# Kernel optimization log

Measured on AMD Instinct MI355X. Metric: run time of the kernel, lower is better.

Reference implementation:

```python
import jax, jax.numpy as jnp
import numpy as np

DIM = 256
FFN_DIM = 512
NH = 8
EPS = 1e-5


def ln(x, g, b):
    m = x.mean(-1, keepdims=True)
    v = ((x - m) ** 2).mean(-1, keepdims=True)
    return (x - m) / jnp.sqrt(v + EPS) * g + b


def setup_inputs() -> dict:
    key = jax.random.key(0)
    ks = jax.random.split(key, 16)
    B, L, C, H, W = 16, 16384, DIM, 128, 128
    s = 0.02
    return {
        "query": jax.random.normal(ks[0], (B, 1, C), jnp.float32),
        "mem": jax.random.normal(ks[1], (B, L, C), jnp.float32),
        "ior_emb": jax.random.uniform(ks[2], (B, NH, H, W), jnp.float32),
        # input_proj: Linear(dim,dim) + ReLU + LayerNorm
        "W_ip": jax.random.normal(ks[3], (C, C), jnp.float32) * s,
        "b_ip": jnp.zeros((C,), jnp.float32),
        "g_ip": jnp.ones((C,), jnp.float32),
        "be_ip": jnp.zeros((C,), jnp.float32),
        # q / kv projections
        "W_q": jax.random.normal(ks[4], (C, C), jnp.float32) * s,
        "b_q": jnp.zeros((C,), jnp.float32),
        "W_kv": jax.random.normal(ks[5], (C, 2 * C), jnp.float32) * s,
        "b_kv": jnp.zeros((2 * C,), jnp.float32),
        # norm_q, norm_ffn
        "g_q": jnp.ones((C,), jnp.float32),
        "be_q": jnp.zeros((C,), jnp.float32),
        "g_f": jnp.ones((C,), jnp.float32),
        "be_f": jnp.zeros((C,), jnp.float32),
        # ffn (Mlp)
        "W1": jax.random.normal(ks[6], (C, FFN_DIM), jnp.float32) * s,
        "b1": jnp.zeros((FFN_DIM,), jnp.float32),
        "W2": jax.random.normal(ks[7], (FFN_DIM, C), jnp.float32) * s,
        "b2": jnp.zeros((C,), jnp.float32),
    }


def reference(query, mem, ior_emb, W_ip, b_ip, g_ip, be_ip, W_q, b_q, W_kv, b_kv,
              g_q, be_q, g_f, be_f, W1, b1, W2, b2):
    B, L, C = mem.shape
    nh = ior_emb.shape[1]
    hd = C // nh
    scale = hd ** -0.5
    # input_proj(mem): Linear -> ReLU -> LayerNorm
    m = ln(jax.nn.relu(mem @ W_ip + b_ip), g_ip, be_ip)  # [B,L,C]
    kv = m @ W_kv + b_kv
    k, v = kv[..., :C], kv[..., C:]
    q = ln(query, g_q, be_q) @ W_q + b_q  # [B,1,C]
    # per-head split along channel == reshape (..., nh, hd)
    qh = q.reshape(B, 1, nh, hd)
    kh = k.reshape(B, L, nh, hd)
    vh = v.reshape(B, L, nh, hd)
    ior = ior_emb.reshape(B, nh, 1, L)
    scores = jnp.einsum('bqhd,blhd->bhql', qh, kh) * scale * ior  # [B,nh,1,L]
    attn = jax.nn.softmax(scores, axis=-1)
    out = jnp.einsum('bhql,blhd->bqhd', attn, vh).reshape(B, 1, C)
    x = out + query
    h = ln(x, g_f, be_f)
    ffn = jax.nn.gelu(h @ W1 + b1, approximate=False) @ W2 + b2
    return x + ffn
```

## Files before the change

kernel.cpp:

```cpp
#include <hip/hip_runtime.h>
#include <math.h>

#define CDIM 256
#define LDIM 16384
#define NH 8
#define HD 32
#define FFN 512
#define EPS 1e-5f
#define SCALE 0.17677669529663687f

#define RB 64
#define CHUNKS (LDIM/RB)
#define LDA 264

typedef __attribute__((ext_vector_type(8))) short short8;
typedef __attribute__((ext_vector_type(4))) float f32x4;

__device__ inline unsigned short f2bf(float x) {
    unsigned int u = __float_as_uint(x);
    unsigned int lsb = (u >> 16) & 1u;
    u += 0x7fffu + lsb;
    return (unsigned short)(u >> 16);
}


__global__ __launch_bounds__(256) void convert_weights(const float* __restrict__ Wip,
                                                       const float* __restrict__ Wkv,
                                                       unsigned short* __restrict__ w1,
                                                       unsigned short* __restrict__ wkv) {
    int idx = blockIdx.x * 256 + threadIdx.x;
    if (idx < 65536) {
        int j = idx & 7, l = (idx >> 3) & 63, c = (idx >> 9) & 15, t = idx >> 13;
        int k = t * 32 + (l >> 4) * 8 + j;
        int col = c * 16 + (l & 15);
        w1[idx] = f2bf(Wip[k * CDIM + col]);
    }
    if (idx < 131072) {
        int j = idx & 7, l = (idx >> 3) & 63, c = (idx >> 9) & 31, t = idx >> 14;
        int k = t * 32 + (l >> 4) * 8 + j;
        int col = c * 16 + (l & 15);
        wkv[idx] = f2bf(Wkv[k * 2 * CDIM + col]);
    }
}


__global__ __launch_bounds__(256) void qprep_kernel(const float* __restrict__ query,
                                                    const float* __restrict__ Wq,
                                                    const float* __restrict__ bq,
                                                    const float* __restrict__ gq,
                                                    const float* __restrict__ beq,
                                                    float* __restrict__ qs) {
    int b = blockIdx.x;
    int tid = threadIdx.x;
    int wave = tid >> 6, lane = tid & 63;
    __shared__ float sh[CDIM];
    __shared__ float red[8];

    float x = query[b * CDIM + tid];
    float s = x, sq = x * x;
#pragma unroll
    for (int m = 32; m >= 1; m >>= 1) { s += __shfl_xor(s, m, 64); sq += __shfl_xor(sq, m, 64); }
    if (lane == 0) { red[wave] = s; red[4 + wave] = sq; }
    __syncthreads();
    float ts = red[0] + red[1] + red[2] + red[3];
    float tq = red[4] + red[5] + red[6] + red[7];
    float mean = ts * (1.f / CDIM);
    float var = tq * (1.f / CDIM) - mean * mean;
    float rstd = rsqrtf(var + EPS);
    sh[tid] = (x - mean) * rstd * gq[tid] + beq[tid];
    __syncthreads();

    float acc = bq[tid];
    for (int k = 0; k < CDIM; ++k) acc = fmaf(sh[k], Wq[k * CDIM + tid], acc);
    qs[b * CDIM + tid] = acc * SCALE;
}


__device__ inline void mfma_gemm(const unsigned short* __restrict__ smA,
                                 const unsigned short* __restrict__ wsw, int NC, int ctile0,
                                 int lx, int quad, f32x4 acc[4][4]) {
#pragma unroll
    for (int rt = 0; rt < 4; ++rt)
#pragma unroll
        for (int ci = 0; ci < 4; ++ci) acc[rt][ci] = (f32x4){0.f, 0.f, 0.f, 0.f};

    int l = quad * 16 + lx;
#pragma unroll
    for (int t = 0; t < 8; ++t) {
        short8 bfrag[4];
#pragma unroll
        for (int ci = 0; ci < 4; ++ci)
            bfrag[ci] = *(const short8*)(wsw + (((size_t)(t * NC + ctile0 + ci)) * 64 + l) * 8);
        short8 afrag[4];
#pragma unroll
        for (int rt = 0; rt < 4; ++rt)
            afrag[rt] = *(const short8*)(smA + (rt * 16 + lx) * LDA + t * 32 + quad * 8);
#pragma unroll
        for (int rt = 0; rt < 4; ++rt)
#pragma unroll
            for (int ci = 0; ci < 4; ++ci)
                acc[rt][ci] = __builtin_amdgcn_mfma_f32_16x16x32_bf16(afrag[rt], bfrag[ci], acc[rt][ci], 0, 0, 0);
    }
}


__global__ __launch_bounds__(256, 2) void main_kernel(const float* __restrict__ mem,
                                                      const unsigned short* __restrict__ w1,
                                                      const unsigned short* __restrict__ wkv,
                                                      const float* __restrict__ bip,
                                                      const float* __restrict__ gip,
                                                      const float* __restrict__ beip,
                                                      const float* __restrict__ bkv,
                                                      const float* __restrict__ ior,
                                                      const float* __restrict__ qs,
                                                      float* __restrict__ partials) {
    int blk = blockIdx.x;
    int b = blk / CHUNKS;
    int chunk = blk % CHUNKS;
    int row0 = chunk * RB;
    int tid = threadIdx.x;
    int w = tid >> 6, l = tid & 63;
    int quad = l >> 4, lx = l & 15;

    __shared__ unsigned short bufA[RB * LDA];
    __shared__ float iorS[NH][RB];
    __shared__ float redS[4][RB];
    __shared__ float redQ[4][RB];
    __shared__ float stats[2][RB];

    {
        int i0 = tid, i1 = tid + 256;
        int h0 = i0 >> 6, r0 = i0 & 63;
        int h1 = i1 >> 6, r1 = i1 & 63;
        iorS[h0][r0] = ior[((size_t)(b * NH + h0)) * LDIM + row0 + r0];
        iorS[h1][r1] = ior[((size_t)(b * NH + h1)) * LDIM + row0 + r1];
    }
    {
        const float4* src = (const float4*)(mem + ((size_t)b * LDIM + row0) * CDIM);
#pragma unroll
        for (int it = 0; it < 16; ++it) {
            int i = tid + 256 * it;
            int r = i >> 6, c4 = i & 63;
            float4 v = src[i];
            ushort4 u;
            u.x = f2bf(v.x); u.y = f2bf(v.y); u.z = f2bf(v.z); u.w = f2bf(v.w);
            *(ushort4*)&bufA[r * LDA + c4 * 4] = u;
        }
    }
    __syncthreads();

    int col[4];
#pragma unroll
    for (int ci = 0; ci < 4; ++ci) col[ci] = (4 * w + ci) * 16 + lx;

    f32x4 acc[4][4];
    mfma_gemm(bufA, w1, 16, 4 * w, lx, quad, acc);

    float bb[4], gg[4], ee[4];
#pragma unroll
    for (int ci = 0; ci < 4; ++ci) { bb[ci] = bip[col[ci]]; gg[ci] = gip[col[ci]]; ee[ci] = beip[col[ci]]; }

#pragma unroll
    for (int rt = 0; rt < 4; ++rt) {
#pragma unroll
        for (int reg = 0; reg < 4; ++reg) {
#pragma unroll
            for (int ci = 0; ci < 4; ++ci)
                acc[rt][ci][reg] = fmaxf(acc[rt][ci][reg] + bb[ci], 0.f);
            float s = acc[rt][0][reg] + acc[rt][1][reg] + acc[rt][2][reg] + acc[rt][3][reg];
            float q = acc[rt][0][reg] * acc[rt][0][reg] + acc[rt][1][reg] * acc[rt][1][reg]
                    + acc[rt][2][reg] * acc[rt][2][reg] + acc[rt][3][reg] * acc[rt][3][reg];
#pragma unroll
            for (int m = 8; m >= 1; m >>= 1) { s += __shfl_xor(s, m, 64); q += __shfl_xor(q, m, 64); }
            if (lx == 0) {
                int row = rt * 16 + quad * 4 + reg;
                redS[w][row] = s;
                redQ[w][row] = q;
            }
        }
    }
    __syncthreads();
    if (tid < RB) {
        float s = redS[0][tid] + redS[1][tid] + redS[2][tid] + redS[3][tid];
        float q = redQ[0][tid] + redQ[1][tid] + redQ[2][tid] + redQ[3][tid];
        float mean = s * (1.f / CDIM);
        float var = q * (1.f / CDIM) - mean * mean;
        stats[0][tid] = mean;
        stats[1][tid] = rsqrtf(var + EPS);
    }
    __syncthreads();

#pragma unroll
    for (int rt = 0; rt < 4; ++rt)
#pragma unroll
        for (int reg = 0; reg < 4; ++reg) {
            int row = rt * 16 + quad * 4 + reg;
            float mean = stats[0][row], rstd = stats[1][row];
#pragma unroll
            for (int ci = 0; ci < 4; ++ci) {
                float y = (acc[rt][ci][reg] - mean) * rstd * gg[ci] + ee[ci];
                bufA[row * LDA + col[ci]] = f2bf(y);
            }
        }
    __syncthreads();

    f32x4 acc2[4][4];
    mfma_gemm(bufA, wkv, 32, 4 * w, lx, quad, acc2);

    float qv[4], bk[4];
#pragma unroll
    for (int ci = 0; ci < 4; ++ci) { qv[ci] = qs[b * CDIM + col[ci]]; bk[ci] = bkv[col[ci]]; }

    float p0[16], p1[16];
    float M0 = -1e30f, M1 = -1e30f;
#pragma unroll
    for (int rt = 0; rt < 4; ++rt)
#pragma unroll
        for (int reg = 0; reg < 4; ++reg) {
            float s0 = (acc2[rt][0][reg] + bk[0]) * qv[0] + (acc2[rt][1][reg] + bk[1]) * qv[1];
            float s1 = (acc2[rt][2][reg] + bk[2]) * qv[2] + (acc2[rt][3][reg] + bk[3]) * qv[3];
#pragma unroll
            for (int m = 8; m >= 1; m >>= 1) { s0 += __shfl_xor(s0, m, 64); s1 += __shfl_xor(s1, m, 64); }
            int row = rt * 16 + quad * 4 + reg;
            s0 *= iorS[2 * w][row];
            s1 *= iorS[2 * w + 1][row];
            p0[rt * 4 + reg] = s0;
            p1[rt * 4 + reg] = s1;
            M0 = fmaxf(M0, s0);
            M1 = fmaxf(M1, s1);
        }
    M0 = fmaxf(M0, __shfl_xor(M0, 16, 64)); M0 = fmaxf(M0, __shfl_xor(M0, 32, 64));
    M1 = fmaxf(M1, __shfl_xor(M1, 16, 64)); M1 = fmaxf(M1, __shfl_xor(M1, 32, 64));
    float S0 = 0.f, S1 = 0.f;
#pragma unroll
    for (int i = 0; i < 16; ++i) {
        p0[i] = __expf(p0[i] - M0); S0 += p0[i];
        p1[i] = __expf(p1[i] - M1); S1 += p1[i];
    }
    S0 += __shfl_xor(S0, 16, 64); S0 += __shfl_xor(S0, 32, 64);
    S1 += __shfl_xor(S1, 16, 64); S1 += __shfl_xor(S1, 32, 64);

    f32x4 acc3[4][4];
    mfma_gemm(bufA, wkv, 32, 16 + 4 * w, lx, quad, acc3);

    float o[4];
#pragma unroll
    for (int ci = 0; ci < 4; ++ci) {
        float bo = bkv[CDIM + col[ci]];
        const float* pp = (ci < 2) ? p0 : p1;
        float a = 0.f;
#pragma unroll
        for (int rt = 0; rt < 4; ++rt)
#pragma unroll
            for (int reg = 0; reg < 4; ++reg)
                a = fmaf(pp[rt * 4 + reg], acc3[rt][ci][reg] + bo, a);
        a += __shfl_xor(a, 16, 64);
        a += __shfl_xor(a, 32, 64);
        o[ci] = a;
    }

    float* P0 = &partials[((size_t)blk * NH + 2 * w) * 34];
    float* P1 = P0 + 34;
    if (quad == 0) {
        P0[2 + lx] = o[0];
        P0[2 + 16 + lx] = o[1];
        P1[2 + lx] = o[2];
        P1[2 + 16 + lx] = o[3];
        if (lx == 0) { P0[0] = M0; P0[1] = S0; P1[0] = M1; P1[1] = S1; }
    }
}


__global__ __launch_bounds__(64) void combine_kernel(const float* __restrict__ partials,
                                                     float* __restrict__ attnout) {
    int bh = blockIdx.x;
    int b = bh >> 3, h = bh & 7;
    int lane = threadIdx.x;

    float M = -1e30f;
    for (int c = lane; c < CHUNKS; c += 64)
        M = fmaxf(M, partials[(((size_t)b * CHUNKS + c) * NH + h) * 34]);
#pragma unroll
    for (int m = 32; m >= 1; m >>= 1) M = fmaxf(M, __shfl_xor(M, m, 64));

    float S = 0.f;
    for (int c = lane; c < CHUNKS; c += 64) {
        const float* P = &partials[(((size_t)b * CHUNKS + c) * NH + h) * 34];
        S += P[1] * __expf(P[0] - M);
    }
#pragma unroll
    for (int m = 32; m >= 1; m >>= 1) S += __shfl_xor(S, m, 64);

    int d = lane & 31, half = lane >> 5;
    float O = 0.f;
    for (int c = half; c < CHUNKS; c += 2) {
        const float* P = &partials[(((size_t)b * CHUNKS + c) * NH + h) * 34];
        O = fmaf(P[2 + d], __expf(P[0] - M), O);
    }
    O += __shfl_xor(O, 32, 64);
    if (lane < 32) attnout[b * CDIM + h * HD + d] = O / S;
}


__global__ __launch_bounds__(256) void epilogue_kernel(const float* __restrict__ attnout,
                                                       const float* __restrict__ query,
                                                       const float* __restrict__ gf,
                                                       const float* __restrict__ bef,
                                                       const float* __restrict__ W1,
                                                       const float* __restrict__ b1,
                                                       const float* __restrict__ W2,
                                                       const float* __restrict__ b2,
                                                       float* __restrict__ out) {
    int b = blockIdx.x;
    int tid = threadIdx.x;
    int wave = tid >> 6, lane = tid & 63;
    __shared__ float sh[FFN];
    __shared__ float red[8];

    float x = attnout[b * CDIM + tid] + query[b * CDIM + tid];
    float s = x, sq = x * x;
#pragma unroll
    for (int m = 32; m >= 1; m >>= 1) { s += __shfl_xor(s, m, 64); sq += __shfl_xor(sq, m, 64); }
    if (lane == 0) { red[wave] = s; red[4 + wave] = sq; }
    __syncthreads();
    float ts = red[0] + red[1] + red[2] + red[3];
    float tq = red[4] + red[5] + red[6] + red[7];
    float mean = ts * (1.f / CDIM);
    float var = tq * (1.f / CDIM) - mean * mean;
    float rstd = rsqrtf(var + EPS);
    sh[tid] = (x - mean) * rstd * gf[tid] + bef[tid];
    __syncthreads();

    float t[2];
#pragma unroll
    for (int i = 0; i < 2; ++i) {
        int f = tid + 256 * i;
        float a = b1[f];
        for (int k = 0; k < CDIM; ++k) a = fmaf(sh[k], W1[k * FFN + f], a);
        t[i] = 0.5f * a * (1.f + erff(a * 0.7071067811865476f));
    }
    __syncthreads();
    sh[tid] = t[0];
    sh[tid + 256] = t[1];
    __syncthreads();

    float y = b2[tid];
    for (int f = 0; f < FFN; ++f) y = fmaf(sh[f], W2[f * CDIM + tid], y);
    out[b * CDIM + tid] = x + y;
}


extern "C" void kernel_launch(void* const* d_in, const int* in_sizes, int n_in,
                              void* d_out, int out_size, void* d_ws, size_t ws_size,
                              hipStream_t stream) {
    const float* query = (const float*)d_in[0];
    const float* mem   = (const float*)d_in[1];
    const float* ior   = (const float*)d_in[2];
    const float* Wip   = (const float*)d_in[3];
    const float* bip   = (const float*)d_in[4];
    const float* gip   = (const float*)d_in[5];
    const float* beip  = (const float*)d_in[6];
    const float* Wq    = (const float*)d_in[7];
    const float* bq    = (const float*)d_in[8];
    const float* Wkv   = (const float*)d_in[9];
    const float* bkv   = (const float*)d_in[10];
    const float* gq    = (const float*)d_in[11];
    const float* beq   = (const float*)d_in[12];
    const float* gf    = (const float*)d_in[13];
    const float* bef   = (const float*)d_in[14];
    const float* W1    = (const float*)d_in[15];
    const float* b1    = (const float*)d_in[16];
    const float* W2    = (const float*)d_in[17];
    const float* b2    = (const float*)d_in[18];
    float* out = (float*)d_out;

    char* ws = (char*)d_ws;
    float* qs             = (float*)(ws);
    float* attnout        = (float*)(ws + 16384);
    float* partials       = (float*)(ws + 32768);
    unsigned short* w1sw  = (unsigned short*)(ws + 32768 + 4456448);
    unsigned short* wkvsw = (unsigned short*)(ws + 32768 + 4456448 + 131072);

    const int B = 16;

    convert_weights<<<512, 256, 0, stream>>>(Wip, Wkv, w1sw, wkvsw);
    qprep_kernel<<<B, 256, 0, stream>>>(query, Wq, bq, gq, beq, qs);
    main_kernel<<<B * CHUNKS, 256, 0, stream>>>(mem, w1sw, wkvsw, bip, gip, beip, bkv, ior, qs, partials);
    combine_kernel<<<B * NH, 64, 0, stream>>>(partials, attnout);
    epilogue_kernel<<<B, 256, 0, stream>>>(attnout, query, gf, bef, W1, b1, W2, b2, out);
}
```

Before: 611.3 us.

## Halve rows per block, fuse K and V GEMMs, merge prep kernels

Cuts rows per block from 64 to 32, doubling the block count and raising launch bounds to 3 blocks per CU for better occupancy on the memory-bound main kernel. The K and V projection GEMMs are merged into one loop so the A fragments from shared memory are read once for both. Weight conversion and query prep are combined into one launch, and the partials workspace is doubled. The cost is that each block now reloads the full weight fragments for half as many rows, doubling weight traffic per row, and more partials have to be combined.

```diff
diff --git a/kernel.cpp b/kernel.cpp
--- a/kernel.cpp
+++ b/kernel.cpp
@@ -9,7 +9,7 @@
 #define EPS 1e-5f
 #define SCALE 0.17677669529663687f
 
-#define RB 64
+#define RB 32
 #define CHUNKS (LDIM/RB)
 #define LDA 264
 
@@ -24,87 +24,59 @@
 }
 
 
-__global__ __launch_bounds__(256) void convert_weights(const float* __restrict__ Wip,
-                                                       const float* __restrict__ Wkv,
-                                                       unsigned short* __restrict__ w1,
-                                                       unsigned short* __restrict__ wkv) {
-    int idx = blockIdx.x * 256 + threadIdx.x;
-    if (idx < 65536) {
-        int j = idx & 7, l = (idx >> 3) & 63, c = (idx >> 9) & 15, t = idx >> 13;
-        int k = t * 32 + (l >> 4) * 8 + j;
-        int col = c * 16 + (l & 15);
-        w1[idx] = f2bf(Wip[k * CDIM + col]);
-    }
-    if (idx < 131072) {
-        int j = idx & 7, l = (idx >> 3) & 63, c = (idx >> 9) & 31, t = idx >> 14;
-        int k = t * 32 + (l >> 4) * 8 + j;
-        int col = c * 16 + (l & 15);
-        wkv[idx] = f2bf(Wkv[k * 2 * CDIM + col]);
-    }
-}
-
-
-__global__ __launch_bounds__(256) void qprep_kernel(const float* __restrict__ query,
-                                                    const float* __restrict__ Wq,
-                                                    const float* __restrict__ bq,
-                                                    const float* __restrict__ gq,
-                                                    const float* __restrict__ beq,
-                                                    float* __restrict__ qs) {
-    int b = blockIdx.x;
-    int tid = threadIdx.x;
-    int wave = tid >> 6, lane = tid & 63;
-    __shared__ float sh[CDIM];
-    __shared__ float red[8];
-
-    float x = query[b * CDIM + tid];
-    float s = x, sq = x * x;
-#pragma unroll
-    for (int m = 32; m >= 1; m >>= 1) { s += __shfl_xor(s, m, 64); sq += __shfl_xor(sq, m, 64); }
-    if (lane == 0) { red[wave] = s; red[4 + wave] = sq; }
-    __syncthreads();
-    float ts = red[0] + red[1] + red[2] + red[3];
-    float tq = red[4] + red[5] + red[6] + red[7];
-    float mean = ts * (1.f / CDIM);
-    float var = tq * (1.f / CDIM) - mean * mean;
-    float rstd = rsqrtf(var + EPS);
-    sh[tid] = (x - mean) * rstd * gq[tid] + beq[tid];
-    __syncthreads();
-
-    float acc = bq[tid];
-    for (int k = 0; k < CDIM; ++k) acc = fmaf(sh[k], Wq[k * CDIM + tid], acc);
-    qs[b * CDIM + tid] = acc * SCALE;
-}
-
-
-__device__ inline void mfma_gemm(const unsigned short* __restrict__ smA,
-                                 const unsigned short* __restrict__ wsw, int NC, int ctile0,
-                                 int lx, int quad, f32x4 acc[4][4]) {
-#pragma unroll
-    for (int rt = 0; rt < 4; ++rt)
-#pragma unroll
-        for (int ci = 0; ci < 4; ++ci) acc[rt][ci] = (f32x4){0.f, 0.f, 0.f, 0.f};
-
-    int l = quad * 16 + lx;
-#pragma unroll
-    for (int t = 0; t < 8; ++t) {
-        short8 bfrag[4];
-#pragma unroll
-        for (int ci = 0; ci < 4; ++ci)
-            bfrag[ci] = *(const short8*)(wsw + (((size_t)(t * NC + ctile0 + ci)) * 64 + l) * 8);
-        short8 afrag[4];
-#pragma unroll
-        for (int rt = 0; rt < 4; ++rt)
-            afrag[rt] = *(const short8*)(smA + (rt * 16 + lx) * LDA + t * 32 + quad * 8);
-#pragma unroll
-        for (int rt = 0; rt < 4; ++rt)
-#pragma unroll
-            for (int ci = 0; ci < 4; ++ci)
-                acc[rt][ci] = __builtin_amdgcn_mfma_f32_16x16x32_bf16(afrag[rt], bfrag[ci], acc[rt][ci], 0, 0, 0);
-    }
-}
-
-
-__global__ __launch_bounds__(256, 2) void main_kernel(const float* __restrict__ mem,
+__global__ __launch_bounds__(256) void prep_kernel(const float* __restrict__ Wip,
+                                                   const float* __restrict__ Wkv,
+                                                   unsigned short* __restrict__ w1,
+                                                   unsigned short* __restrict__ wkv,
+                                                   const float* __restrict__ query,
+                                                   const float* __restrict__ Wq,
+                                                   const float* __restrict__ bq,
+                                                   const float* __restrict__ gq,
+                                                   const float* __restrict__ beq,
+                                                   float* __restrict__ qs) {
+    if (blockIdx.x < 512) {
+        int idx = blockIdx.x * 256 + threadIdx.x;
+        if (idx < 65536) {
+            int j = idx & 7, l = (idx >> 3) & 63, c = (idx >> 9) & 15, t = idx >> 13;
+            int k = t * 32 + (l >> 4) * 8 + j;
+            int col = c * 16 + (l & 15);
+            w1[idx] = f2bf(Wip[k * CDIM + col]);
+        }
+        {
+            int j = idx & 7, l = (idx >> 3) & 63, c = (idx >> 9) & 31, t = idx >> 14;
+            int k = t * 32 + (l >> 4) * 8 + j;
+            int col = c * 16 + (l & 15);
+            wkv[idx] = f2bf(Wkv[k * 2 * CDIM + col]);
+        }
+    } else {
+        int b = blockIdx.x - 512;
+        int tid = threadIdx.x;
+        int wave = tid >> 6, lane = tid & 63;
+        __shared__ float sh[CDIM];
+        __shared__ float red[8];
+
+        float x = query[b * CDIM + tid];
+        float s = x, sq = x * x;
+#pragma unroll
+        for (int m = 32; m >= 1; m >>= 1) { s += __shfl_xor(s, m, 64); sq += __shfl_xor(sq, m, 64); }
+        if (lane == 0) { red[wave] = s; red[4 + wave] = sq; }
+        __syncthreads();
+        float ts = red[0] + red[1] + red[2] + red[3];
+        float tq = red[4] + red[5] + red[6] + red[7];
+        float mean = ts * (1.f / CDIM);
+        float var = tq * (1.f / CDIM) - mean * mean;
+        float rstd = rsqrtf(var + EPS);
+        sh[tid] = (x - mean) * rstd * gq[tid] + beq[tid];
+        __syncthreads();
+
+        float acc = bq[tid];
+        for (int k = 0; k < CDIM; ++k) acc = fmaf(sh[k], Wq[k * CDIM + tid], acc);
+        qs[b * CDIM + tid] = acc * SCALE;
+    }
+}
+
+
+__global__ __launch_bounds__(256, 3) void main_kernel(const float* __restrict__ mem,
                                                       const unsigned short* __restrict__ w1,
                                                       const unsigned short* __restrict__ wkv,
                                                       const float* __restrict__ bip,
@@ -129,16 +101,13 @@
     __shared__ float stats[2][RB];
 
     {
-        int i0 = tid, i1 = tid + 256;
-        int h0 = i0 >> 6, r0 = i0 & 63;
-        int h1 = i1 >> 6, r1 = i1 & 63;
+        int h0 = tid >> 5, r0 = tid & 31;
         iorS[h0][r0] = ior[((size_t)(b * NH + h0)) * LDIM + row0 + r0];
-        iorS[h1][r1] = ior[((size_t)(b * NH + h1)) * LDIM + row0 + r1];
     }
     {
         const float4* src = (const float4*)(mem + ((size_t)b * LDIM + row0) * CDIM);
 #pragma unroll
-        for (int it = 0; it < 16; ++it) {
+        for (int it = 0; it < 8; ++it) {
             int i = tid + 256 * it;
             int r = i >> 6, c4 = i & 63;
             float4 v = src[i];
@@ -153,15 +122,34 @@
 #pragma unroll
     for (int ci = 0; ci < 4; ++ci) col[ci] = (4 * w + ci) * 16 + lx;
 
-    f32x4 acc[4][4];
-    mfma_gemm(bufA, w1, 16, 4 * w, lx, quad, acc);
+    f32x4 acc[2][4];
+#pragma unroll
+    for (int rt = 0; rt < 2; ++rt)
+#pragma unroll
+        for (int ci = 0; ci < 4; ++ci) acc[rt][ci] = (f32x4){0.f, 0.f, 0.f, 0.f};
+#pragma unroll
+    for (int t = 0; t < 8; ++t) {
+        short8 bfrag[4];
+#pragma unroll
+        for (int ci = 0; ci < 4; ++ci)
+            bfrag[ci] = *(const short8*)(w1 + (((size_t)(t * 16 + 4 * w + ci)) * 64 + l) * 8);
+        short8 afrag[2];
+#pragma unroll
+        for (int rt = 0; rt < 2; ++rt)
+            afrag[rt] = *(const short8*)(bufA + (rt * 16 + lx) * LDA + t * 32 + quad * 8);
+#pragma unroll
+        for (int rt = 0; rt < 2; ++rt)
+#pragma unroll
+            for (int ci = 0; ci < 4; ++ci)
+                acc[rt][ci] = __builtin_amdgcn_mfma_f32_16x16x32_bf16(afrag[rt], bfrag[ci], acc[rt][ci], 0, 0, 0);
+    }
 
     float bb[4], gg[4], ee[4];
 #pragma unroll
     for (int ci = 0; ci < 4; ++ci) { bb[ci] = bip[col[ci]]; gg[ci] = gip[col[ci]]; ee[ci] = beip[col[ci]]; }
 
 #pragma unroll
-    for (int rt = 0; rt < 4; ++rt) {
+    for (int rt = 0; rt < 2; ++rt) {
 #pragma unroll
         for (int reg = 0; reg < 4; ++reg) {
 #pragma unroll
@@ -191,7 +179,7 @@
     __syncthreads();
 
 #pragma unroll
-    for (int rt = 0; rt < 4; ++rt)
+    for (int rt = 0; rt < 2; ++rt)
 #pragma unroll
         for (int reg = 0; reg < 4; ++reg) {
             int row = rt * 16 + quad * 4 + reg;
@@ -204,17 +192,43 @@
         }
     __syncthreads();
 
-    f32x4 acc2[4][4];
-    mfma_gemm(bufA, wkv, 32, 4 * w, lx, quad, acc2);
+    f32x4 acc2[2][4], acc3[2][4];
+#pragma unroll
+    for (int rt = 0; rt < 2; ++rt)
+#pragma unroll
+        for (int ci = 0; ci < 4; ++ci) {
+            acc2[rt][ci] = (f32x4){0.f, 0.f, 0.f, 0.f};
+            acc3[rt][ci] = (f32x4){0.f, 0.f, 0.f, 0.f};
+        }
+#pragma unroll
+    for (int t = 0; t < 8; ++t) {
+        short8 bfragK[4], bfragV[4];
+#pragma unroll
+        for (int ci = 0; ci < 4; ++ci) {
+            bfragK[ci] = *(const short8*)(wkv + (((size_t)(t * 32 + 4 * w + ci)) * 64 + l) * 8);
+            bfragV[ci] = *(const short8*)(wkv + (((size_t)(t * 32 + 16 + 4 * w + ci)) * 64 + l) * 8);
+        }
+        short8 afrag[2];
+#pragma unroll
+        for (int rt = 0; rt < 2; ++rt)
+            afrag[rt] = *(const short8*)(bufA + (rt * 16 + lx) * LDA + t * 32 + quad * 8);
+#pragma unroll
+        for (int rt = 0; rt < 2; ++rt)
+#pragma unroll
+            for (int ci = 0; ci < 4; ++ci) {
+                acc2[rt][ci] = __builtin_amdgcn_mfma_f32_16x16x32_bf16(afrag[rt], bfragK[ci], acc2[rt][ci], 0, 0, 0);
+                acc3[rt][ci] = __builtin_amdgcn_mfma_f32_16x16x32_bf16(afrag[rt], bfragV[ci], acc3[rt][ci], 0, 0, 0);
+            }
+    }
 
     float qv[4], bk[4];
 #pragma unroll
     for (int ci = 0; ci < 4; ++ci) { qv[ci] = qs[b * CDIM + col[ci]]; bk[ci] = bkv[col[ci]]; }
 
-    float p0[16], p1[16];
+    float p0[8], p1[8];
     float M0 = -1e30f, M1 = -1e30f;
 #pragma unroll
-    for (int rt = 0; rt < 4; ++rt)
+    for (int rt = 0; rt < 2; ++rt)
 #pragma unroll
         for (int reg = 0; reg < 4; ++reg) {
             float s0 = (acc2[rt][0][reg] + bk[0]) * qv[0] + (acc2[rt][1][reg] + bk[1]) * qv[1];
@@ -233,15 +247,12 @@
     M1 = fmaxf(M1, __shfl_xor(M1, 16, 64)); M1 = fmaxf(M1, __shfl_xor(M1, 32, 64));
     float S0 = 0.f, S1 = 0.f;
 #pragma unroll
-    for (int i = 0; i < 16; ++i) {
+    for (int i = 0; i < 8; ++i) {
         p0[i] = __expf(p0[i] - M0); S0 += p0[i];
         p1[i] = __expf(p1[i] - M1); S1 += p1[i];
     }
     S0 += __shfl_xor(S0, 16, 64); S0 += __shfl_xor(S0, 32, 64);
     S1 += __shfl_xor(S1, 16, 64); S1 += __shfl_xor(S1, 32, 64);
-
-    f32x4 acc3[4][4];
-    mfma_gemm(bufA, wkv, 32, 16 + 4 * w, lx, quad, acc3);
 
     float o[4];
 #pragma unroll
@@ -250,7 +261,7 @@
         const float* pp = (ci < 2) ? p0 : p1;
         float a = 0.f;
 #pragma unroll
-        for (int rt = 0; rt < 4; ++rt)
+        for (int rt = 0; rt < 2; ++rt)
 #pragma unroll
             for (int reg = 0; reg < 4; ++reg)
                 a = fmaf(pp[rt * 4 + reg], acc3[rt][ci][reg] + bo, a);
@@ -378,13 +389,12 @@
     float* qs             = (float*)(ws);
     float* attnout        = (float*)(ws + 16384);
     float* partials       = (float*)(ws + 32768);
-    unsigned short* w1sw  = (unsigned short*)(ws + 32768 + 4456448);
-    unsigned short* wkvsw = (unsigned short*)(ws + 32768 + 4456448 + 131072);
+    unsigned short* w1sw  = (unsigned short*)(ws + 32768 + 8912896);
+    unsigned short* wkvsw = (unsigned short*)(ws + 32768 + 8912896 + 131072);
 
     const int B = 16;
 
-    convert_weights<<<512, 256, 0, stream>>>(Wip, Wkv, w1sw, wkvsw);
-    qprep_kernel<<<B, 256, 0, stream>>>(query, Wq, bq, gq, beq, qs);
+    prep_kernel<<<512 + B, 256, 0, stream>>>(Wip, Wkv, w1sw, wkvsw, query, Wq, bq, gq, beq, qs);
     main_kernel<<<B * CHUNKS, 256, 0, stream>>>(mem, w1sw, wkvsw, bip, gip, beip, bkv, ior, qs, partials);
     combine_kernel<<<B * NH, 64, 0, stream>>>(partials, attnout);
     epilogue_kernel<<<B, 256, 0, stream>>>(attnout, query, gf, bef, W1, b1, W2, b2, out);
```

Result: no change. 616.0 us (+0.8%).
